# Performance work log

Measured on AMD Instinct MI355X. Metric: run time of the kernel, lower is better.

Reference implementation:

```python
import jax, jax.numpy as jnp
import numpy as np

B, N, H = 16, 1024, 1024


def setup_inputs() -> dict:
    key = jax.random.key(0)
    ks = jax.random.split(key, 12)
    inv = 1.0 / np.sqrt(H)
    inp = {
        "x": jax.random.normal(ks[0], (B, N, H), jnp.float32),
        "atom_graph": jax.random.normal(ks[1], (B, N, N), jnp.float32),
        "variable_graph": jax.random.normal(ks[2], (B, N, N), jnp.float32),
        "Wq": jax.random.uniform(ks[3], (H, H), jnp.float32, -inv, inv),
        "bq": jax.random.uniform(ks[4], (H,), jnp.float32, -inv, inv),
        "Wk": jax.random.uniform(ks[5], (H, H), jnp.float32, -inv, inv),
        "bk": jax.random.uniform(ks[6], (H,), jnp.float32, -inv, inv),
        "Wv": jax.random.uniform(ks[7], (H, H), jnp.float32, -inv, inv),
        "bv": jax.random.uniform(ks[8], (H,), jnp.float32, -inv, inv),
        "predicate_pos": jax.random.randint(ks[9], (B, N), 0, 2, jnp.int32),
        "variable_tags": jax.random.randint(ks[10], (B, N), 0, 4, jnp.int32),
    }
    return inp


def _path_pool(h, predicate_pos):
    # h: [B,N,H]; predicate_pos: [B,N] in {0,1}
    b, n, d = h.shape
    i = jnp.arange(n)
    # pos[i-2] (value irrelevant for i<2, those branches handled explicitly)
    pp2 = jnp.pad(predicate_pos, ((0, 0), (2, 0)))[:, :n]  # [B,N]
    # window [s, e): i==0 -> [0,2); i==1 -> [0,3); pos[i-2]==1 -> [i,i+2); else [i-1,i+2)
    s = jnp.where(i < 2, 0, jnp.where(pp2 == 1, i, i - 1))  # [B,N]
    e = jnp.where(i == 0, 2, jnp.where(i == 1, 3, i + 2))    # [N]
    e = jnp.minimum(e, n)
    e = jnp.broadcast_to(e, (b, n))
    # prefix sums along node dim with a leading zero row -> windowed means via gather
    cs = jnp.concatenate([jnp.zeros((b, 1, d), h.dtype), jnp.cumsum(h, axis=1)], axis=1)  # [B,N+1,H]
    win_sum = (jnp.take_along_axis(cs, e[:, :, None], axis=1)
               - jnp.take_along_axis(cs, s[:, :, None], axis=1))  # [B,N,H]
    means = win_sum / (e - s)[:, :, None].astype(h.dtype)
    mask = (predicate_pos == 1).astype(h.dtype)  # [B,N]
    item = (means * mask[:, :, None]).sum(axis=1) / mask.sum(axis=1)[:, None]  # [B,H]
    return jnp.broadcast_to(item[:, None, :], (b, n, d))


def reference(x, atom_graph, variable_graph, Wq, bq, Wk, bk, Wv, bv,
              predicate_pos, variable_tags):
    scale = x.shape[-1] ** (-0.5)
    q = (x @ Wq.T + bq) * scale
    k = x @ Wk.T + bk
    v = x @ Wv.T + bv
    att = jnp.einsum("bnh,bmh->bnm", q, k) + atom_graph + variable_graph
    att = jax.nn.softmax(att, axis=-1)  # dropout is identity in eval
    h = jnp.einsum("bnm,bmh->bnh", att, v)
    return _path_pool(h, predicate_pos)
```

## Files before the change

kernel.cpp:

```cpp
#include <hip/hip_runtime.h>
#include <hip/hip_bf16.h>

#define BATCH 16
#define SEQ   1024
#define DIM   1024

typedef __attribute__((ext_vector_type(8))) short bf16x8;
typedef __attribute__((ext_vector_type(4))) float f32x4;
typedef __attribute__((ext_vector_type(4))) unsigned short us4;

__device__ __forceinline__ float bfu2f(unsigned short u) {
  union { unsigned int i; float f; } c; c.i = ((unsigned int)u) << 16; return c.f;
}
__device__ __forceinline__ unsigned short f2bfu(float f) {
  union { float f; unsigned int i; } c; c.f = f;
  return (unsigned short)((c.i + 0x7FFFu + ((c.i >> 16) & 1u)) >> 16);
}
__device__ __forceinline__ void async16(void* lds, const void* g) {
  __builtin_amdgcn_global_load_lds(
      (const __attribute__((address_space(1))) unsigned int*)g,
      (__attribute__((address_space(3))) unsigned int*)lds, 16, 0, 0);
}

__global__ void cast_xw_kernel(const float* __restrict__ x, const float* __restrict__ Wv,
                               unsigned short* __restrict__ xb,
                               unsigned short* __restrict__ Wvb, int x4) {
  int i = blockIdx.x * blockDim.x + threadIdx.x;
  const float* in; unsigned short* out; int j;
  if (i < x4) { in = x; out = xb; j = i; }
  else { in = Wv; out = Wvb; j = i - x4; }
  f32x4 v = ((const f32x4*)in)[j];
  us4 o;
  o[0] = f2bfu(v[0]); o[1] = f2bfu(v[1]); o[2] = f2bfu(v[2]); o[3] = f2bfu(v[3]);
  ((us4*)out)[j] = o;
}

__global__ void castT_kernel(const float* __restrict__ Wq, const float* __restrict__ Wk,
                             unsigned short* __restrict__ WqT,
                             unsigned short* __restrict__ WkT) {
  const float* in = (blockIdx.z == 0) ? Wq : Wk;
  unsigned short* out = (blockIdx.z == 0) ? WqT : WkT;
  __shared__ float t[64][65];
  const int h0 = blockIdx.x * 64, i0 = blockIdx.y * 64;
  const int tid = threadIdx.x;
  const int sub = tid >> 4, c4 = tid & 15;
#pragma unroll
  for (int p = 0; p < 4; ++p) {
    const int row = p * 16 + sub;
    f32x4 v = *(const f32x4*)(in + (size_t)(h0 + row) * DIM + i0 + c4 * 4);
    t[row][c4 * 4 + 0] = v[0]; t[row][c4 * 4 + 1] = v[1];
    t[row][c4 * 4 + 2] = v[2]; t[row][c4 * 4 + 3] = v[3];
  }
  __syncthreads();
#pragma unroll
  for (int p = 0; p < 4; ++p) {
    const int orow = p * 16 + sub;
    us4 o;
    o[0] = f2bfu(t[c4 * 4 + 0][orow]);
    o[1] = f2bfu(t[c4 * 4 + 1][orow]);
    o[2] = f2bfu(t[c4 * 4 + 2][orow]);
    o[3] = f2bfu(t[c4 * 4 + 3][orow]);
    *(us4*)(out + (size_t)(i0 + orow) * DIM + h0 + c4 * 4) = o;
  }
}

__global__ void t12_kernel(const unsigned short* __restrict__ WqT,
                           const unsigned short* __restrict__ WkT,
                           const float* __restrict__ bq, const float* __restrict__ bk,
                           float* __restrict__ t1, float* __restrict__ t2) {
  const int y = blockIdx.y;
  const unsigned short* Wt = y ? WkT : WqT;
  const float* vec = y ? bq : bk;
  float* tout = y ? t2 : t1;
  const int wave = threadIdx.x >> 6, lane = threadIdx.x & 63;
  const int i = blockIdx.x * 4 + wave;
  const us4* wr = (const us4*)(Wt + (size_t)i * DIM);
  float s = 0.f;
#pragma unroll
  for (int t = 0; t < 4; ++t) {
    us4 w4 = wr[lane + 64 * t];
    f32x4 b4 = *(const f32x4*)(vec + (lane + 64 * t) * 4);
    s += bfu2f(w4[0]) * b4[0] + bfu2f(w4[1]) * b4[1] +
         bfu2f(w4[2]) * b4[2] + bfu2f(w4[3]) * b4[3];
  }
#pragma unroll
  for (int o = 32; o; o >>= 1) s += __shfl_down(s, o);
  if (lane == 0) tout[i] = s;
}

__global__ void ac_kernel(const unsigned short* __restrict__ xb,
                          const float* __restrict__ t1, const float* __restrict__ t2,
                          const float* __restrict__ bq, const float* __restrict__ bk,
                          float* __restrict__ a, float* __restrict__ c) {
  const float scale = 0.03125f;
  const int tid = threadIdx.x;
  const int wave = tid >> 6, lane = tid & 63;
  float dp = 0.f;
  for (int i = tid; i < DIM; i += 256) dp += bq[i] * bk[i];
#pragma unroll
  for (int o = 32; o; o >>= 1) dp += __shfl_down(dp, o);
  __shared__ float dred[4];
  if ((tid & 63) == 0) dred[tid >> 6] = dp;
  __syncthreads();
  const float d = dred[0] + dred[1] + dred[2] + dred[3];
  float t1r[16], t2r[16];
#pragma unroll
  for (int t = 0; t < 4; ++t) {
    f32x4 v1 = *(const f32x4*)(t1 + (lane + 64 * t) * 4);
    f32x4 v2 = *(const f32x4*)(t2 + (lane + 64 * t) * 4);
#pragma unroll
    for (int j = 0; j < 4; ++j) { t1r[t * 4 + j] = v1[j]; t2r[t * 4 + j] = v2[j]; }
  }
  for (int rr = 0; rr < 16; ++rr) {
    const int row = blockIdx.x * 64 + wave * 16 + rr;
    const us4* xr = (const us4*)(xb + (size_t)row * DIM);
    float sa = 0.f, sc = 0.f;
#pragma unroll
    for (int t = 0; t < 4; ++t) {
      us4 v = xr[lane + 64 * t];
#pragma unroll
      for (int j = 0; j < 4; ++j) {
        const float f = bfu2f(v[j]);
        sa += f * t1r[t * 4 + j];
        sc += f * t2r[t * 4 + j];
      }
    }
#pragma unroll
    for (int o = 32; o; o >>= 1) { sa += __shfl_down(sa, o); sc += __shfl_down(sc, o); }
    if (lane == 0) {
      a[row] = scale * (sa + d);
      c[row] = scale * sc;
    }
  }
}

__global__ void pathw_kernel(const int* __restrict__ pos, float* __restrict__ w,
                             float* __restrict__ zbias) {
  const int b = blockIdx.x;
  __shared__ int ps[SEQ];
  __shared__ int mcnt;
  const int tid = threadIdx.x;
  if (tid == 0) mcnt = 0;
  __syncthreads();
  if (b == 0)
    for (int i = tid; i < DIM; i += 256) zbias[i] = 0.f;
  for (int i = tid; i < SEQ; i += 256) ps[i] = pos[b * SEQ + i];
  __syncthreads();
  int c = 0;
  for (int i = tid; i < SEQ; i += 256) c += ps[i];
  for (int o = 32; o; o >>= 1) c += __shfl_down(c, o);
  if ((tid & 63) == 0) atomicAdd(&mcnt, c);
  __syncthreads();
  const float invM = 1.0f / (float)mcnt;
  for (int j = tid; j < SEQ; j += 256) {
    float a = 0.f;
#pragma unroll
    for (int di = -1; di <= 1; ++di) {
      int i = j + di;
      if (i < 0 || i >= SEQ) continue;
      if (!ps[i]) continue;
      int s, e;
      if (i < 2) { s = 0; e = (i == 0) ? 2 : 3; }
      else { s = (ps[i - 2] == 1) ? i : (i - 1); e = i + 2; if (e > SEQ) e = SEQ; }
      if (s <= j && j < e) a += 1.0f / (float)(e - s);
    }
    w[b * SEQ + j] = a * invM;
  }
}

__global__ void proj_gemm(const unsigned short* __restrict__ A,
                          const unsigned short* __restrict__ W,
                          const float* __restrict__ bias, float alpha,
                          unsigned short* __restrict__ C, int M, int N, int K)
{
  __shared__ __align__(16) char smem[32768];
  float* Sl = (float*)smem;
  const int tid = threadIdx.x;
  const int wave = tid >> 6, lane = tid & 63;
  const int lr = lane & 15, lg = lane >> 4;
  const int wr = wave >> 1, wc = wave & 1;
  const int m0 = blockIdx.x * 128, n0 = blockIdx.y * 128;
  const int off0 = tid * 16, off1 = 4096 + tid * 16;
  const int r0 = off0 >> 6, ke0 = (off0 >> 1) & 31;
  const int r1 = off1 >> 6, ke1 = (off1 >> 1) & 31;
  f32x4 acc[4][4] = {};

  auto stage = [&](char* base, int kk) {
    async16(base + off0, A + (size_t)(m0 + r0) * K + kk + ke0);
    async16(base + off1, A + (size_t)(m0 + r1) * K + kk + ke1);
    async16(base + 8192 + off0, W + (size_t)(n0 + r0) * K + kk + ke0);
    async16(base + 8192 + off1, W + (size_t)(n0 + r1) * K + kk + ke1);
  };
  auto compute = [&](const char* base) {
    bf16x8 af[4], bfv[4];
#pragma unroll
    for (int i = 0; i < 4; ++i) {
      af[i]  = *(const bf16x8*)(base + ((wr * 64 + i * 16 + lr) << 6) + (lg << 4));
      bfv[i] = *(const bf16x8*)(base + 8192 + ((wc * 64 + i * 16 + lr) << 6) + (lg << 4));
    }
#pragma unroll
    for (int i = 0; i < 4; ++i)
#pragma unroll
      for (int j = 0; j < 4; ++j)
        acc[i][j] = __builtin_amdgcn_mfma_f32_16x16x32_bf16(af[i], bfv[j], acc[i][j], 0, 0, 0);
  };

  const int nt = K >> 5;
  stage(smem, 0);
  __syncthreads();
  int cur = 0;
  for (int k = 0; k < nt - 1; ++k) {
    stage(smem + ((cur ^ 1) << 14), (k + 1) << 5);
    compute(smem + (cur << 14));
    __syncthreads();
    cur ^= 1;
  }
  compute(smem + (cur << 14));
#pragma unroll
  for (int p = 0; p < 4; ++p) {
    __syncthreads();
    if (wr == (p >> 1)) {
      const int ibase = (p & 1) * 2;
#pragma unroll
      for (int ii = 0; ii < 2; ++ii) {
        const int i = ibase + ii;
#pragma unroll
        for (int j = 0; j < 4; ++j)
#pragma unroll
          for (int r = 0; r < 4; ++r)
            Sl[(ii * 16 + lg * 4 + r) * 132 + wc * 64 + j * 16 + lr] = acc[i][j][r];
      }
    }
    __syncthreads();
#pragma unroll
    for (int it = 0; it < 4; ++it) {
      const int v = tid + it * 256;
      const int lrow = v >> 5, c4 = v & 31;
      const int grow = m0 + p * 32 + lrow;
      const int col = n0 + c4 * 4;
      const f32x4 s4 = *(const f32x4*)(&Sl[lrow * 132 + c4 * 4]);
      const f32x4 b4 = *(const f32x4*)(bias + col);
      us4 o;
      o[0] = f2bfu((s4[0] + b4[0]) * alpha);
      o[1] = f2bfu((s4[1] + b4[1]) * alpha);
      o[2] = f2bfu((s4[2] + b4[2]) * alpha);
      o[3] = f2bfu((s4[3] + b4[3]) * alpha);
      *(us4*)(C + (size_t)grow * N + col) = o;
    }
  }
}

__global__ __launch_bounds__(512, 2)
void gemm256(const unsigned short* __restrict__ A,
             const unsigned short* __restrict__ B,
             unsigned short* __restrict__ C)
{
  extern __shared__ __align__(16) char smem[];
  const size_t boff = (size_t)blockIdx.z << 20;
  const int m0 = blockIdx.y * 256, n0 = blockIdx.x * 256;
  const int tid = threadIdx.x;
  const int lane = tid & 63;
  const int wid = tid >> 6;
  const int wm = wid >> 2, wn = wid & 3;
  const int lr = lane & 15, lg = lane >> 4;
  const unsigned short* Ab = A + boff;
  const unsigned short* Bb = B + boff;

  int sr[2], se[2], sL[2];
#pragma unroll
  for (int l = 0; l < 2; ++l) {
    const int L = l * 8192 + tid * 16;
    const int r = L >> 6, sp = (L >> 4) & 3;
    sL[l] = L; sr[l] = r; se[l] = (sp ^ ((r >> 1) & 3)) * 8;
  }
  int aoff[8], boff_[4];
#pragma unroll
  for (int i = 0; i < 8; ++i) {
    const int row = wm * 128 + i * 16 + lr;
    aoff[i] = row * 64 + (lg ^ ((row >> 1) & 3)) * 16;
  }
#pragma unroll
  for (int j = 0; j < 4; ++j) {
    const int row = wn * 64 + j * 16 + lr;
    boff_[j] = row * 64 + (lg ^ ((row >> 1) & 3)) * 16;
  }

  auto stage = [&](int slot, int kt) {
    char* sa = smem + slot * 32768;
#pragma unroll
    for (int l = 0; l < 2; ++l)
      async16(sa + sL[l], Ab + (size_t)(m0 + sr[l]) * DIM + kt * 32 + se[l]);
    char* sb = sa + 16384;
#pragma unroll
    for (int l = 0; l < 2; ++l)
      async16(sb + sL[l], Bb + (size_t)(n0 + sr[l]) * DIM + kt * 32 + se[l]);
  };

  f32x4 acc[8][4] = {};
  stage(0, 0); stage(1, 1); stage(2, 2); stage(3, 3);

#pragma unroll
  for (int t = 0; t < 32; ++t) {
    if (t == 0)       asm volatile("s_waitcnt vmcnt(12)" ::: "memory");
    else if (t <= 29) asm volatile("s_waitcnt vmcnt(8)" ::: "memory");
    else if (t == 30) asm volatile("s_waitcnt vmcnt(4)" ::: "memory");
    else              asm volatile("s_waitcnt vmcnt(0)" ::: "memory");
    __builtin_amdgcn_s_barrier();
    if (t >= 1 && t <= 28) stage((t + 3) & 3, t + 3);
    const char* sa = smem + (t & 3) * 32768;
    const char* sb = sa + 16384;
    bf16x8 a[8], bfr[4];
#pragma unroll
    for (int i = 0; i < 8; ++i) a[i] = *(const bf16x8*)(sa + aoff[i]);
#pragma unroll
    for (int j = 0; j < 4; ++j) bfr[j] = *(const bf16x8*)(sb + boff_[j]);
    __builtin_amdgcn_s_setprio(1);
#pragma unroll
    for (int i = 0; i < 8; ++i)
#pragma unroll
      for (int j = 0; j < 4; ++j)
        acc[i][j] = __builtin_amdgcn_mfma_f32_16x16x32_bf16(a[i], bfr[j], acc[i][j], 0, 0, 0);
    __builtin_amdgcn_s_setprio(0);
  }

  unsigned short* Sl = (unsigned short*)smem;
  unsigned short* Cb = C + boff;
#pragma unroll
  for (int half = 0; half < 2; ++half) {
    __syncthreads();
    if (wm == half) {
#pragma unroll
      for (int i = 0; i < 8; ++i)
#pragma unroll
        for (int j = 0; j < 4; ++j)
#pragma unroll
          for (int r = 0; r < 4; ++r)
            Sl[(i * 16 + lg * 4 + r) * 260 + wn * 64 + j * 16 + lr] =
                f2bfu(acc[i][j][r]);
    }
    __syncthreads();
#pragma unroll
    for (int it = 0; it < 16; ++it) {
      const int v = tid + it * 512;
      const int row = v >> 6, c4 = v & 63;
      *(us4*)(Cb + (size_t)(m0 + half * 128 + row) * SEQ + n0 + c4 * 4) =
          *(const us4*)(&Sl[row * 260 + c4 * 4]);
    }
  }
}

__global__ void exp_fused_kernel(const unsigned short* __restrict__ S,
                                 const float* __restrict__ ag, const float* __restrict__ vg,
                                 const float* __restrict__ av, const float* __restrict__ cv,
                                 const float* __restrict__ w, float* __restrict__ part)
{
  __shared__ float red[4][SEQ];
  const int b = blockIdx.y;
  const int tid = threadIdx.x;
  const int wave = tid >> 6, lane = tid & 63;
  const float* agb = ag + ((size_t)b << 20);
  const float* vgb = vg + ((size_t)b << 20);
  const unsigned short* Sb = S + ((size_t)b << 20);
  const float* cvb = cv + b * SEQ;
  f32x4 cq[4];
#pragma unroll
  for (int qi = 0; qi < 4; ++qi)
    cq[qi] = *(const f32x4*)(cvb + (lane + 64 * qi) * 4);
  f32x4 ur[4] = {};
  const int r0 = blockIdx.x * 8 + wave * 2;
  const float w0 = w[b * SEQ + r0];
  const float w1 = w[b * SEQ + r0 + 1];
  us4 sv[2][4]; f32x4 a4[2][4], g4[2][4];
#pragma unroll
  for (int r = 0; r < 2; ++r) {
    const float wr_ = r ? w1 : w0;
    if (wr_ == 0.f) continue;
    const int row = r0 + r;
#pragma unroll
    for (int qi = 0; qi < 4; ++qi) {
      const size_t base = (size_t)row * SEQ + (lane + 64 * qi) * 4;
      sv[r][qi] = *(const us4*)(Sb + base);
      a4[r][qi] = *(const f32x4*)(agb + base);
      g4[r][qi] = *(const f32x4*)(vgb + base);
    }
  }
#pragma unroll
  for (int r = 0; r < 2; ++r) {
    const float wr_ = r ? w1 : w0;
    if (wr_ == 0.f) continue;
    const int row = r0 + r;
    const float arow = av[b * SEQ + row];
    float e[16];
    float rs = 0.f;
#pragma unroll
    for (int qi = 0; qi < 4; ++qi)
#pragma unroll
      for (int j = 0; j < 4; ++j) {
        const float ev = __expf(bfu2f(sv[r][qi][j]) + a4[r][qi][j] + g4[r][qi][j] +
                                arow + cq[qi][j]);
        e[qi * 4 + j] = ev;
        rs += ev;
      }
#pragma unroll
    for (int o2 = 32; o2; o2 >>= 1) rs += __shfl_xor(rs, o2);
    const float cn = wr_ / rs;
#pragma unroll
    for (int qi = 0; qi < 4; ++qi)
#pragma unroll
      for (int j = 0; j < 4; ++j)
        ur[qi][j] += cn * e[qi * 4 + j];
  }
#pragma unroll
  for (int qi = 0; qi < 4; ++qi)
    *(f32x4*)(&red[wave][(lane + 64 * qi) * 4]) = ur[qi];
  __syncthreads();
  const int col = tid * 4;
  f32x4 s0 = *(const f32x4*)(&red[0][col]);
  const f32x4 s1 = *(const f32x4*)(&red[1][col]);
  const f32x4 s2 = *(const f32x4*)(&red[2][col]);
  const f32x4 s3 = *(const f32x4*)(&red[3][col]);
  s0[0] += s1[0] + s2[0] + s3[0];
  s0[1] += s1[1] + s2[1] + s3[1];
  s0[2] += s1[2] + s2[2] + s3[2];
  s0[3] += s1[3] + s2[3] + s3[3];
  *(f32x4*)(part + ((size_t)(b * 128 + blockIdx.x) << 10) + col) = s0;
}

__global__ void wcol_kernel(const unsigned short* __restrict__ Mt,
                            const float* __restrict__ wv,
                            const float* __restrict__ pin,
                            float* __restrict__ part) {
  const int nc = blockIdx.x;
  const int b = blockIdx.y;
  const int tid = threadIdx.x;
  __shared__ float c[64];
  if (pin) {
    const int n = nc * 64 + (tid & 63);
    const int bl0 = (tid >> 6) * 32;
    float s = 0.f;
#pragma unroll 8
    for (int bl = 0; bl < 32; ++bl)
      s += pin[((size_t)(b * 128 + bl0 + bl) << 10) + n];
    __shared__ float cp[4][64];
    cp[tid >> 6][tid & 63] = s;
    __syncthreads();
    if (tid < 64) c[tid] = cp[0][tid] + cp[1][tid] + cp[2][tid] + cp[3][tid];
  } else {
    if (tid < 64) c[tid] = wv[b * SEQ + nc * 64 + tid];
  }
  __syncthreads();
  const unsigned short* p = Mt + ((size_t)b << 20) + ((size_t)(nc * 64) << 10) + tid * 4;
  f32x4 acc = {0.f, 0.f, 0.f, 0.f};
#pragma unroll 8
  for (int n = 0; n < 64; ++n) {
    const us4 v = *(const us4*)(p + ((size_t)n << 10));
    const float cn = c[n];
    acc[0] += cn * bfu2f(v[0]); acc[1] += cn * bfu2f(v[1]);
    acc[2] += cn * bfu2f(v[2]); acc[3] += cn * bfu2f(v[3]);
  }
  *(f32x4*)(part + (size_t)((b * 16 + nc) << 10) + tid * 4) = acc;
}

__global__ void wred_kernel(const float* __restrict__ part, float* __restrict__ vec,
                            int nchunks) {
  const int b = blockIdx.x;
  const int tid = threadIdx.x;
  f32x4 s = {0.f, 0.f, 0.f, 0.f};
  for (int nc = 0; nc < nchunks; ++nc) {
    const f32x4 v = *(const f32x4*)(part + ((size_t)(b * nchunks + nc) << 10) + tid * 4);
    s[0] += v[0]; s[1] += v[1]; s[2] += v[2]; s[3] += v[3];
  }
  *(f32x4*)(vec + b * SEQ + tid * 4) = s;
}

__global__ void item_kernel(const float* __restrict__ y,
                            const unsigned short* __restrict__ Wvb,
                            const float* __restrict__ bv, float* __restrict__ item) {
  const int b = blockIdx.x;
  const int hblk = blockIdx.y;
  __shared__ float ys[DIM];
  const int tid = threadIdx.x;
  for (int i = tid; i < DIM; i += 256) ys[i] = y[b * DIM + i];
  __syncthreads();
  const int wave = tid >> 6, lane = tid & 63;
  const int h = hblk * 4 + wave;
  const us4* wrow = (const us4*)(Wvb + (size_t)h * DIM);
  float acc = 0.f;
#pragma unroll
  for (int t = 0; t < 4; ++t) {
    us4 v = wrow[t * 64 + lane];
    const int d0 = (t * 64 + lane) * 4;
    acc += ys[d0] * bfu2f(v[0]) + ys[d0 + 1] * bfu2f(v[1]) +
           ys[d0 + 2] * bfu2f(v[2]) + ys[d0 + 3] * bfu2f(v[3]);
  }
  for (int o = 32; o; o >>= 1) acc += __shfl_down(acc, o);
  if (lane == 0) item[b * DIM + h] = acc + bv[h];
}

__global__ void bcast_kernel(const float* __restrict__ item, float* __restrict__ out) {
  const int b = blockIdx.y;
  const int n = blockIdx.x;
  const f32x4* src = (const f32x4*)(item + b * DIM);
  f32x4* dst = (f32x4*)(out + (((size_t)b * SEQ + n) << 10));
  dst[threadIdx.x] = src[threadIdx.x];
}

extern "C" void kernel_launch(void* const* d_in, const int* in_sizes, int n_in,
                              void* d_out, int out_size, void* d_ws, size_t ws_size,
                              hipStream_t stream) {
  const float* x    = (const float*)d_in[0];
  const float* ag   = (const float*)d_in[1];
  const float* vgr  = (const float*)d_in[2];
  const float* Wq   = (const float*)d_in[3];
  const float* bq   = (const float*)d_in[4];
  const float* Wk   = (const float*)d_in[5];
  const float* bk   = (const float*)d_in[6];
  const float* Wv   = (const float*)d_in[7];
  const float* bv   = (const float*)d_in[8];
  const int*   pos  = (const int*)d_in[9];
  float* out = (float*)d_out;

  char* ws = (char*)d_ws;
  size_t off = 0;
  auto alloc = [&](size_t bytes) { void* p = ws + off; off += (bytes + 255) & ~(size_t)255; return p; };
  const size_t BNH = (size_t)BATCH * SEQ * DIM;
  unsigned short* xb   = (unsigned short*)alloc(BNH * 2);
  unsigned short* zb   = (unsigned short*)alloc(BNH * 2);
  unsigned short* S    = (unsigned short*)alloc(BNH * 2);
  unsigned short* WqT  = (unsigned short*)alloc((size_t)DIM * DIM * 2);
  unsigned short* WkT  = (unsigned short*)alloc((size_t)DIM * DIM * 2);
  unsigned short* Wvb  = (unsigned short*)alloc((size_t)DIM * DIM * 2);
  unsigned short* Hb   = (unsigned short*)alloc((size_t)DIM * DIM * 2);
  float* w     = (float*)alloc((size_t)BATCH * SEQ * 4);
  float* av    = (float*)alloc((size_t)BATCH * SEQ * 4);
  float* cvv   = (float*)alloc((size_t)BATCH * SEQ * 4);
  float* t1    = (float*)alloc((size_t)DIM * 4);
  float* t2    = (float*)alloc((size_t)DIM * 4);
  float* zbias = (float*)alloc((size_t)DIM * 4);
  float* y     = (float*)alloc((size_t)BATCH * DIM * 4);
  float* item  = (float*)alloc((size_t)BATCH * DIM * 4);
  float* partU = (float*)alloc((size_t)BATCH * 128 * SEQ * 4);
  float* partY = (float*)alloc((size_t)BATCH * 16 * SEQ * 4);

  const float scale = 0.03125f;
  const int x4 = (int)(BNH / 4);

  (void)hipFuncSetAttribute(reinterpret_cast<const void*>(gemm256),
                            hipFuncAttributeMaxDynamicSharedMemorySize, 131072);

  cast_xw_kernel<<<(x4 + DIM * DIM / 4) / 256, 256, 0, stream>>>(x, Wv, xb, Wvb, x4);
  castT_kernel<<<dim3(16, 16, 2), 256, 0, stream>>>(Wq, Wk, WqT, WkT);

  pathw_kernel<<<BATCH, 256, 0, stream>>>(pos, w, zbias);

  t12_kernel<<<dim3(256, 2), 256, 0, stream>>>(WqT, WkT, bq, bk, t1, t2);
  ac_kernel<<<256, 256, 0, stream>>>(xb, t1, t2, bq, bk, av, cvv);

  proj_gemm<<<dim3(8, 8), 256, 0, stream>>>(WkT, WqT, zbias, scale, Hb, DIM, DIM, DIM);

  gemm256<<<dim3(4, 64, 1), 512, 131072, stream>>>(xb, Hb, zb);

  gemm256<<<dim3(4, 4, BATCH), 512, 131072, stream>>>(zb, xb, S);

  exp_fused_kernel<<<dim3(128, BATCH), 256, 0, stream>>>(S, ag, vgr, av, cvv, w, partU);

  wcol_kernel<<<dim3(16, BATCH), 256, 0, stream>>>(xb, nullptr, partU, partY);
  wred_kernel<<<BATCH, 256, 0, stream>>>(partY, y, 16);

  item_kernel<<<dim3(BATCH, 256), 256, 0, stream>>>(y, Wvb, bv, item);

  bcast_kernel<<<dim3(SEQ, BATCH), 256, 0, stream>>>(item, out);
}
```

Baseline: 207.4 us.

## Fuse x cast with row dot products and reorder gemm prefetch after LDS reads

Merges the bf16 cast of x and Wv with the per-row a/c dot-product computation into one row-per-block kernel, so x is read once in fp32 instead of being cast and then reread as bf16. The q/k bias dot product moves into the path-weight kernel and is stored to a scalar buffer. The row sums now use full-precision x rather than the bf16 copy. Separately, in gemm256 the async prefetch of the next stage is issued after the current tile's LDS fragment reads instead of before them.

Measured after the change: 197.0 us. 5.0% less time.

```diff
diff --git a/kernel.cpp b/kernel.cpp
--- a/kernel.cpp
+++ b/kernel.cpp
@@ -20,19 +20,6 @@
   __builtin_amdgcn_global_load_lds(
       (const __attribute__((address_space(1))) unsigned int*)g,
       (__attribute__((address_space(3))) unsigned int*)lds, 16, 0, 0);
-}
-
-__global__ void cast_xw_kernel(const float* __restrict__ x, const float* __restrict__ Wv,
-                               unsigned short* __restrict__ xb,
-                               unsigned short* __restrict__ Wvb, int x4) {
-  int i = blockIdx.x * blockDim.x + threadIdx.x;
-  const float* in; unsigned short* out; int j;
-  if (i < x4) { in = x; out = xb; j = i; }
-  else { in = Wv; out = Wvb; j = i - x4; }
-  f32x4 v = ((const f32x4*)in)[j];
-  us4 o;
-  o[0] = f2bfu(v[0]); o[1] = f2bfu(v[1]); o[2] = f2bfu(v[2]); o[3] = f2bfu(v[3]);
-  ((us4*)out)[j] = o;
 }
 
 __global__ void castT_kernel(const float* __restrict__ Wq, const float* __restrict__ Wk,
@@ -88,64 +75,28 @@
   if (lane == 0) tout[i] = s;
 }
 
-__global__ void ac_kernel(const unsigned short* __restrict__ xb,
-                          const float* __restrict__ t1, const float* __restrict__ t2,
-                          const float* __restrict__ bq, const float* __restrict__ bk,
-                          float* __restrict__ a, float* __restrict__ c) {
-  const float scale = 0.03125f;
-  const int tid = threadIdx.x;
-  const int wave = tid >> 6, lane = tid & 63;
-  float dp = 0.f;
-  for (int i = tid; i < DIM; i += 256) dp += bq[i] * bk[i];
-#pragma unroll
-  for (int o = 32; o; o >>= 1) dp += __shfl_down(dp, o);
-  __shared__ float dred[4];
-  if ((tid & 63) == 0) dred[tid >> 6] = dp;
-  __syncthreads();
-  const float d = dred[0] + dred[1] + dred[2] + dred[3];
-  float t1r[16], t2r[16];
-#pragma unroll
-  for (int t = 0; t < 4; ++t) {
-    f32x4 v1 = *(const f32x4*)(t1 + (lane + 64 * t) * 4);
-    f32x4 v2 = *(const f32x4*)(t2 + (lane + 64 * t) * 4);
-#pragma unroll
-    for (int j = 0; j < 4; ++j) { t1r[t * 4 + j] = v1[j]; t2r[t * 4 + j] = v2[j]; }
-  }
-  for (int rr = 0; rr < 16; ++rr) {
-    const int row = blockIdx.x * 64 + wave * 16 + rr;
-    const us4* xr = (const us4*)(xb + (size_t)row * DIM);
-    float sa = 0.f, sc = 0.f;
-#pragma unroll
-    for (int t = 0; t < 4; ++t) {
-      us4 v = xr[lane + 64 * t];
-#pragma unroll
-      for (int j = 0; j < 4; ++j) {
-        const float f = bfu2f(v[j]);
-        sa += f * t1r[t * 4 + j];
-        sc += f * t2r[t * 4 + j];
-      }
-    }
-#pragma unroll
-    for (int o = 32; o; o >>= 1) { sa += __shfl_down(sa, o); sc += __shfl_down(sc, o); }
-    if (lane == 0) {
-      a[row] = scale * (sa + d);
-      c[row] = scale * sc;
-    }
-  }
-}
-
-__global__ void pathw_kernel(const int* __restrict__ pos, float* __restrict__ w,
-                             float* __restrict__ zbias) {
+__global__ void pathw_kernel(const int* __restrict__ pos,
+                             const float* __restrict__ bq, const float* __restrict__ bk,
+                             float* __restrict__ w, float* __restrict__ zbias,
+                             float* __restrict__ dval) {
   const int b = blockIdx.x;
   __shared__ int ps[SEQ];
   __shared__ int mcnt;
+  __shared__ float dred[4];
   const int tid = threadIdx.x;
   if (tid == 0) mcnt = 0;
   __syncthreads();
-  if (b == 0)
+  if (b == 0) {
     for (int i = tid; i < DIM; i += 256) zbias[i] = 0.f;
+    float dp = 0.f;
+    for (int i = tid; i < DIM; i += 256) dp += bq[i] * bk[i];
+#pragma unroll
+    for (int o = 32; o; o >>= 1) dp += __shfl_down(dp, o);
+    if ((tid & 63) == 0) dred[tid >> 6] = dp;
+  }
   for (int i = tid; i < SEQ; i += 256) ps[i] = pos[b * SEQ + i];
   __syncthreads();
+  if (b == 0 && tid == 0) dval[0] = dred[0] + dred[1] + dred[2] + dred[3];
   int c = 0;
   for (int i = tid; i < SEQ; i += 256) c += ps[i];
   for (int o = 32; o; o >>= 1) c += __shfl_down(c, o);
@@ -165,6 +116,48 @@
       if (s <= j && j < e) a += 1.0f / (float)(e - s);
     }
     w[b * SEQ + j] = a * invM;
+  }
+}
+
+__global__ void cast_row_kernel(const float* __restrict__ x, const float* __restrict__ Wv,
+                                const float* __restrict__ t1, const float* __restrict__ t2,
+                                const float* __restrict__ dval,
+                                unsigned short* __restrict__ xb,
+                                unsigned short* __restrict__ Wvb,
+                                float* __restrict__ av, float* __restrict__ cvv) {
+  const int blk = blockIdx.x;
+  const int tid = threadIdx.x;
+  if (blk >= BATCH * SEQ) {
+    const int row = blk - BATCH * SEQ;
+    const size_t base = (size_t)row * DIM + tid * 4;
+    f32x4 v = *(const f32x4*)(Wv + base);
+    us4 o;
+    o[0] = f2bfu(v[0]); o[1] = f2bfu(v[1]); o[2] = f2bfu(v[2]); o[3] = f2bfu(v[3]);
+    *(us4*)(Wvb + base) = o;
+    return;
+  }
+  const size_t base = (size_t)blk * DIM + tid * 4;
+  f32x4 v = *(const f32x4*)(x + base);
+  us4 o;
+  o[0] = f2bfu(v[0]); o[1] = f2bfu(v[1]); o[2] = f2bfu(v[2]); o[3] = f2bfu(v[3]);
+  *(us4*)(xb + base) = o;
+  const f32x4 q1 = *(const f32x4*)(t1 + tid * 4);
+  const f32x4 q2 = *(const f32x4*)(t2 + tid * 4);
+  float sa = v[0] * q1[0] + v[1] * q1[1] + v[2] * q1[2] + v[3] * q1[3];
+  float sc = v[0] * q2[0] + v[1] * q2[1] + v[2] * q2[2] + v[3] * q2[3];
+#pragma unroll
+  for (int off = 32; off; off >>= 1) {
+    sa += __shfl_down(sa, off);
+    sc += __shfl_down(sc, off);
+  }
+  __shared__ float r1[4], r2[4];
+  const int wave = tid >> 6, lane = tid & 63;
+  if (lane == 0) { r1[wave] = sa; r2[wave] = sc; }
+  __syncthreads();
+  if (tid == 0) {
+    const float scale = 0.03125f;
+    av[blk]  = scale * (r1[0] + r1[1] + r1[2] + r1[3] + dval[0]);
+    cvv[blk] = scale * (r2[0] + r2[1] + r2[2] + r2[3]);
   }
 }
 
@@ -306,7 +299,6 @@
     else if (t == 30) asm volatile("s_waitcnt vmcnt(4)" ::: "memory");
     else              asm volatile("s_waitcnt vmcnt(0)" ::: "memory");
     __builtin_amdgcn_s_barrier();
-    if (t >= 1 && t <= 28) stage((t + 3) & 3, t + 3);
     const char* sa = smem + (t & 3) * 32768;
     const char* sb = sa + 16384;
     bf16x8 a[8], bfr[4];
@@ -314,6 +306,7 @@
     for (int i = 0; i < 8; ++i) a[i] = *(const bf16x8*)(sa + aoff[i]);
 #pragma unroll
     for (int j = 0; j < 4; ++j) bfr[j] = *(const bf16x8*)(sb + boff_[j]);
+    if (t >= 1 && t <= 28) stage((t + 3) & 3, t + 3);
     __builtin_amdgcn_s_setprio(1);
 #pragma unroll
     for (int i = 0; i < 8; ++i)
@@ -537,24 +530,23 @@
   float* t1    = (float*)alloc((size_t)DIM * 4);
   float* t2    = (float*)alloc((size_t)DIM * 4);
   float* zbias = (float*)alloc((size_t)DIM * 4);
+  float* dval  = (float*)alloc(256);
   float* y     = (float*)alloc((size_t)BATCH * DIM * 4);
   float* item  = (float*)alloc((size_t)BATCH * DIM * 4);
   float* partU = (float*)alloc((size_t)BATCH * 128 * SEQ * 4);
   float* partY = (float*)alloc((size_t)BATCH * 16 * SEQ * 4);
 
   const float scale = 0.03125f;
-  const int x4 = (int)(BNH / 4);
 
   (void)hipFuncSetAttribute(reinterpret_cast<const void*>(gemm256),
                             hipFuncAttributeMaxDynamicSharedMemorySize, 131072);
 
-  cast_xw_kernel<<<(x4 + DIM * DIM / 4) / 256, 256, 0, stream>>>(x, Wv, xb, Wvb, x4);
   castT_kernel<<<dim3(16, 16, 2), 256, 0, stream>>>(Wq, Wk, WqT, WkT);
-
-  pathw_kernel<<<BATCH, 256, 0, stream>>>(pos, w, zbias);
-
   t12_kernel<<<dim3(256, 2), 256, 0, stream>>>(WqT, WkT, bq, bk, t1, t2);
-  ac_kernel<<<256, 256, 0, stream>>>(xb, t1, t2, bq, bk, av, cvv);
+  pathw_kernel<<<BATCH, 256, 0, stream>>>(pos, bq, bk, w, zbias, dval);
+
+  cast_row_kernel<<<BATCH * SEQ + DIM, 256, 0, stream>>>(x, Wv, t1, t2, dval,
+                                                         xb, Wvb, av, cvv);
 
   proj_gemm<<<dim3(8, 8), 256, 0, stream>>>(WkT, WqT, zbias, scale, Hb, DIM, DIM, DIM);
 
```
